# Performance work log

Measured on AMD Instinct MI355X. Metric: run time of the kernel, lower is better.

Reference implementation:

```python
import jax, jax.numpy as jnp
import numpy as np

EPS = 1e-5

def mean_std_norm(x):
    # instance norm without affine: per-(B,C) mean/std over spatial dims
    mean = jnp.mean(x, axis=(2, 3), keepdims=True)
    var = jnp.var(x, axis=(2, 3), keepdims=True)
    return (x - mean) / jnp.sqrt(var + EPS)

def conv1x1(x, w, b):
    # x: [B,C,H,W], w: [O,C], b: [O]
    return jnp.einsum('oc,bchw->bohw', w, x) + b[None, :, None, None]

def setup_inputs() -> dict:
    key = jax.random.key(0)
    ks = jax.random.split(key, 9)
    C = 512
    s = 1.0 / np.sqrt(C)
    inp = {
        'content_feat': jax.random.normal(ks[0], (4, C, 64, 64), dtype=jnp.float32),
        'f_w': jax.random.normal(ks[1], (C, C), dtype=jnp.float32) * s,
        'f_b': jnp.zeros((C,), dtype=jnp.float32),
        'g_w': jax.random.normal(ks[2], (C, C), dtype=jnp.float32) * s,
        'g_b': jnp.zeros((C,), dtype=jnp.float32),
        'h_w': jax.random.normal(ks[3], (C, C), dtype=jnp.float32) * s,
        'h_b': jnp.zeros((C,), dtype=jnp.float32),
        'o_w': jax.random.normal(ks[4], (C, C), dtype=jnp.float32) * s,
        'o_b': jnp.zeros((C,), dtype=jnp.float32),
    }
    return inp

def reference(content_feat, f_w, f_b, g_w, g_b, h_w, h_b, o_w, o_b):
    B, C, H, W = content_feat.shape
    HW = H * W
    norm = mean_std_norm(content_feat)
    # f(norm) -> [B, HW, C]; g(norm) -> [B, C, HW]
    F_Fc = conv1x1(norm, f_w, f_b).reshape(B, C, HW).transpose(0, 2, 1)
    G_Fs = conv1x1(norm, g_w, g_b).reshape(B, C, HW)
    energy = jnp.einsum('bnc,bcm->bnm', F_Fc, G_Fs)  # [B, HW, HW]
    attention = jax.nn.softmax(energy, axis=-1)
    H_Fs = conv1x1(content_feat, h_w, h_b).reshape(B, C, HW)
    # out = H_Fs @ attention^T : out[b,c,m] = sum_n H_Fs[b,c,n] * att[b,m,n]
    out = jnp.einsum('bcn,bmn->bcm', H_Fs, attention).reshape(B, C, H, W)
    out = conv1x1(out, o_w, o_b)
    return out + content_feat
```

## Files before the change

kernel.cpp:

```cpp
#include <hip/hip_runtime.h>


typedef __bf16 bf16_t;
typedef _Float16 f16_t;
typedef _Float16 f16x8 __attribute__((ext_vector_type(8)));
typedef float f32x4 __attribute__((ext_vector_type(4)));

#define LOG2E 1.44269504088896340736f

__device__ __forceinline__ void gload16(const void* g, void* l) {
  __builtin_amdgcn_global_load_lds(
      (const __attribute__((address_space(1))) void*)g,
      (__attribute__((address_space(3))) void*)l, 16, 0, 0);
}

#define WAITV14() asm volatile("s_waitcnt vmcnt(14)" ::: "memory")
#define WAITV10() asm volatile("s_waitcnt vmcnt(10)" ::: "memory")
#define WAITL() asm volatile("s_waitcnt lgkmcnt(0)" ::: "memory")
#define SB() __builtin_amdgcn_s_barrier()
#define SCHED0() __builtin_amdgcn_sched_barrier(0)

__global__ void __launch_bounds__(256) stats_k(const float* __restrict__ x,
                                               float* __restrict__ mu,
                                               float* __restrict__ rs) {
  const int bc = blockIdx.x;
  const float4* row = (const float4*)(x + (size_t)bc * 4096);
  float s = 0.f, ss = 0.f;
  for (int i = threadIdx.x; i < 1024; i += 256) {
    float4 v = row[i];
    s += v.x + v.y + v.z + v.w;
    ss += v.x * v.x + v.y * v.y + v.z * v.z + v.w * v.w;
  }
#pragma unroll
  for (int o = 32; o >= 1; o >>= 1) {
    s += __shfl_down(s, o);
    ss += __shfl_down(ss, o);
  }
  __shared__ float as_[4], ass_[4];
  const int w = threadIdx.x >> 6;
  if ((threadIdx.x & 63) == 0) { as_[w] = s; ass_[w] = ss; }
  __syncthreads();
  if (threadIdx.x == 0) {
    float st = as_[0] + as_[1] + as_[2] + as_[3];
    float sst = ass_[0] + ass_[1] + ass_[2] + ass_[3];
    float m = st * (1.f / 4096.f);
    float var = sst * (1.f / 4096.f) - m * m;
    mu[bc] = m;
    rs[bc] = rsqrtf(var + 1e-5f);
  }
}

__global__ void __launch_bounds__(256) wcast2_k(const float* __restrict__ a,
                                                const float* __restrict__ b,
                                                f16_t* __restrict__ dst) {
  const int i = blockIdx.x * 256 + threadIdx.x;
  const int which = i >> 16;
  const int off = i & 65535;
  const float* s = which ? b : a;
  const float4 v = ((const float4*)s)[off];
  alignas(8) f16_t r[4];
  r[0] = (f16_t)v.x; r[1] = (f16_t)v.y; r[2] = (f16_t)v.z; r[3] = (f16_t)v.w;
  *(uint2*)(dst + ((size_t)which << 18) + (size_t)off * 4) = *(const uint2*)r;
}

__global__ void __launch_bounds__(256) mt_k(const float* __restrict__ fw,
                                            const float* __restrict__ gw,
                                            f16_t* __restrict__ Mh) {
  __shared__ float Fs[32][64];
  __shared__ float Gs[32][64];
  const int t = threadIdx.x;
  const int it = blockIdx.x, jt = blockIdx.y;
  float acc[16];
#pragma unroll
  for (int i = 0; i < 16; ++i) acc[i] = 0.f;
  const int jl = t >> 2, ib = (t & 3) * 16;
  const int lr = t >> 4, lc4 = (t & 15) * 4;
  for (int cc = 0; cc < 16; ++cc) {
    __syncthreads();
#pragma unroll
    for (int rep = 0; rep < 2; ++rep) {
      const int r = lr + rep * 16;
      *(float4*)&Fs[r][lc4] = *(const float4*)(fw + (size_t)(cc * 32 + r) * 512 + it * 64 + lc4);
      *(float4*)&Gs[r][lc4] = *(const float4*)(gw + (size_t)(cc * 32 + r) * 512 + jt * 64 + lc4);
    }
    __syncthreads();
#pragma unroll
    for (int c = 0; c < 32; ++c) {
      const float gv = Gs[c][jl];
#pragma unroll
      for (int ii = 0; ii < 16; ++ii) acc[ii] += gv * Fs[c][ib + ii];
    }
  }
  alignas(16) f16_t hi[16];
#pragma unroll
  for (int ii = 0; ii < 16; ++ii) hi[ii] = (f16_t)acc[ii];
  const size_t o = (size_t)(jt * 64 + jl) * 512 + it * 64 + ib;
  *(uint4*)(Mh + o) = *(const uint4*)hi;
  *(uint4*)(Mh + o + 8) = *(const uint4*)(hi + 8);
}

__global__ void __launch_bounds__(256) v_k(const float* __restrict__ gw,
                                           const float* __restrict__ fb,
                                           float* __restrict__ v) {
  const int j = blockIdx.x * 256 + threadIdx.x;
  float s = 0.f;
  for (int c = 0; c < 512; ++c) s += gw[(size_t)c * 512 + j] * fb[c];
  v[j] = s;
}

__global__ void __launch_bounds__(256) u_k(const float* __restrict__ v,
                                           const f16_t* __restrict__ xf,
                                           float* __restrict__ u) {
  const int w = threadIdx.x >> 6, lane = threadIdx.x & 63;
  const int m = blockIdx.x * 4 + w;
  const int b = blockIdx.y;
  const size_t o = ((size_t)b * 4096 + m) * 512 + lane * 8;
  const f16x8 vh = *(const f16x8*)(xf + o);
  const float4 v0 = *(const float4*)(v + lane * 8);
  const float4 v1 = *(const float4*)(v + lane * 8 + 4);
  float s = 0.f;
  const float* vp = &v0.x;
#pragma unroll
  for (int e = 0; e < 4; ++e) s += (float)vh[e] * vp[e];
  const float* vq = &v1.x;
#pragma unroll
  for (int e = 0; e < 4; ++e) s += (float)vh[4 + e] * vq[e];
#pragma unroll
  for (int o2 = 32; o2 >= 1; o2 >>= 1) s += __shfl_down(s, o2);
  if (lane == 0) u[(size_t)b * 4096 + m] = s;
}

__global__ void __launch_bounds__(256) normt_k(const float* __restrict__ x,
                                               const float* __restrict__ mu,
                                               const float* __restrict__ rs,
                                               f16_t* __restrict__ xf,
                                               f16_t* __restrict__ xc) {
  __shared__ float tile[64][65];
  const int t = threadIdx.x;
  const int nt = blockIdx.x, ct = blockIdx.y, b = blockIdx.z;
  const float* src = x + ((size_t)b * 512 + ct * 64) * 4096 + nt * 64;
  {
    const int r = t >> 4, cq = (t & 15) * 4;
#pragma unroll
    for (int it = 0; it < 4; ++it) {
      const int rr = r + it * 16;
      const float4 v = *(const float4*)(src + (size_t)rr * 4096 + cq);
      tile[rr][cq] = v.x; tile[rr][cq + 1] = v.y;
      tile[rr][cq + 2] = v.z; tile[rr][cq + 3] = v.w;
    }
  }
  __syncthreads();
  const int n = t & 63, ch = t >> 6;
  alignas(16) f16_t vf[16], vc[16];
#pragma unroll
  for (int i = 0; i < 16; ++i) {
    const int c = ch * 16 + i;
    const float v = tile[c][n];
    const int gc = b * 512 + ct * 64 + c;
    vc[i] = (f16_t)v;
    vf[i] = (f16_t)((v - mu[gc]) * rs[gc]);
  }
  const size_t o = ((size_t)b * 4096 + nt * 64 + n) * 512 + ct * 64 + ch * 16;
  *(uint4*)(xf + o) = *(const uint4*)vf;
  *(uint4*)(xf + o + 8) = *(const uint4*)(vf + 8);
  *(uint4*)(xc + o) = *(const uint4*)vc;
  *(uint4*)(xc + o + 8) = *(const uint4*)(vc + 8);
}

template <typename OT, int BIAS, bool RESID>
__global__ void __launch_bounds__(256) gemm_k(const f16_t* __restrict__ A,
                                              const f16_t* __restrict__ Bt,
                                              OT* __restrict__ C,
                                              const float* __restrict__ biasM,
                                              const float* __restrict__ biasN,
                                              const float* __restrict__ resid,
                                              long sAb, long sBb, long sCb, int ldC) {
  __shared__ alignas(16) f16_t As[2][128 * 64];
  __shared__ alignas(16) f16_t Bs[2][128 * 64];
  const int t = threadIdx.x;
  const int lane = t & 63;
  const int w = t >> 6;
  const int wr = w >> 1, wc = w & 1;
  const int l15 = lane & 15, lg = lane >> 4;
  const int b = blockIdx.z;
  const int m0 = blockIdx.y * 128, n0 = blockIdx.x * 128;
  const f16_t* Ab = A + (size_t)sAb * b + (size_t)m0 * 512;
  const f16_t* Bb = Bt + (size_t)sBb * b + (size_t)n0 * 512;
  const int srow = t >> 3;
  const int slot = t & 7;

  auto gstage = [&](int pb_, int ks_) {
#pragma unroll
    for (int r_ = 0; r_ < 4; ++r_) {
      const int rr_ = r_ * 32 + srow;
      const size_t go_ = (size_t)rr_ * 512 + ks_ * 64 + ((slot ^ (rr_ & 7)) * 8);
      gload16(Ab + go_, (char*)As[pb_] + r_ * 4096 + w * 1024);
      gload16(Bb + go_, (char*)Bs[pb_] + r_ * 4096 + w * 1024);
    }
  };

  const f32x4 z4 = {0.f, 0.f, 0.f, 0.f};
  f32x4 acc[4][4];
#pragma unroll
  for (int i = 0; i < 4; ++i)
#pragma unroll
    for (int j = 0; j < 4; ++j) acc[i][j] = z4;

  gstage(0, 0);
  __syncthreads();
  for (int ks = 0; ks < 8; ++ks) {
    const int pb = ks & 1;
    if (ks < 7) gstage(pb ^ 1, ks + 1);
#pragma unroll
    for (int kk = 0; kk < 2; ++kk) {
      f16x8 af[4], bfr[4];
#pragma unroll
      for (int i = 0; i < 4; ++i) {
        const int ra = wr * 64 + i * 16 + l15;
        af[i] = *(const f16x8*)((const char*)As[pb] + ra * 128 + (((kk * 4 + lg) ^ (ra & 7)) * 16));
        const int rb = wc * 64 + i * 16 + l15;
        bfr[i] = *(const f16x8*)((const char*)Bs[pb] + rb * 128 + (((kk * 4 + lg) ^ (rb & 7)) * 16));
      }
#pragma unroll
      for (int i = 0; i < 4; ++i)
#pragma unroll
        for (int j = 0; j < 4; ++j)
          acc[i][j] = __builtin_amdgcn_mfma_f32_16x16x32_f16(af[i], bfr[j], acc[i][j], 0, 0, 0);
    }
    __syncthreads();
  }
  OT* Cb = C + (size_t)sCb * b;
#pragma unroll
  for (int i = 0; i < 4; ++i) {
#pragma unroll
    for (int j = 0; j < 4; ++j) {
      const int n = n0 + wc * 64 + j * 16 + l15;
      float bn = 0.f;
      if (BIAS == 2) bn = biasN[n];
#pragma unroll
      for (int r = 0; r < 4; ++r) {
        const int m = m0 + wr * 64 + i * 16 + lg * 4 + r;
        float v = acc[i][j][r] + bn;
        if (BIAS == 1) v += biasM[m];
        if (RESID) v += resid[(size_t)sCb * b + (size_t)m * ldC + n];
        Cb[(size_t)m * ldC + n] = (OT)v;
      }
    }
  }
}

__global__ void __launch_bounds__(512, 2) flash_k(const f16_t* __restrict__ Z,
                                                  const f16_t* __restrict__ X,
                                                  const float* __restrict__ u,
                                                  const f16_t* __restrict__ Hv,
                                                  f16_t* __restrict__ Oat_t) {
  __shared__ alignas(16) f16_t K[2][64 * 256];
  __shared__ alignas(16) f16_t P[64 * 72];
  __shared__ float redm[4][2][16];
  __shared__ float reds[4][2][16];
  __shared__ float alds[64];
  __shared__ float llds[64];

  const int t = threadIdx.x;
  const int lane = t & 63;
  const int w = t >> 6;
  const int wq = w & 3, wk = w >> 2;
  const int l15 = lane & 15, lg = lane >> 4;
  const int bid = blockIdx.x;
  const int xcd = bid & 7;
  const int b = xcd >> 1;
  const int q0 = ((xcd & 1) * 32 + (bid >> 3)) * 64;

  const f16_t* Kb = X + (size_t)b * 4096 * 512;
  const f16_t* Vb = Hv + (size_t)b * 512 * 4096;
  const float* ub = u + (size_t)b * 4096;

  const int srow = w * 2 + (lane >> 5);
  const int slot32 = lane & 31;

  auto stagek = [&](int pb_, int kt_, int hf_) {
    const int k0_ = kt_ * 64;
#pragma unroll
    for (int r_ = 0; r_ < 4; ++r_) {
      const int row_ = r_ * 16 + srow;
      const size_t go_ = (size_t)(k0_ + row_) * 512 + hf_ * 256 + ((slot32 ^ (row_ & 7)) * 8);
      gload16(Kb + go_, (char*)K[pb_] + r_ * 8192 + w * 1024);
    }
  };

#define QKHALF(PB, HF)                                                                        \
  do {                                                                                        \
    _Pragma("unroll") for (int cwl_ = 0; cwl_ < 8; ++cwl_) {                                  \
      const f16x8 qf_ = qf[(HF) * 8 + cwl_];                                                  \
      _Pragma("unroll") for (int mf_ = 0; mf_ < 2; ++mf_) {                                   \
        const int key_ = 32 * wk + 16 * mf_ + l15;                                            \
        const int so_ = ((cwl_ * 4 + lg) ^ (key_ & 7)) * 16;                                  \
        const f16x8 kf_ = *(const f16x8*)((const char*)K[PB] + key_ * 512 + so_);             \
        sacc[mf_] = __builtin_amdgcn_mfma_f32_16x16x32_f16(kf_, qf_, sacc[mf_], 0, 0, 0);     \
      }                                                                                       \
    }                                                                                         \
  } while (0)

  f16x8 qf[16];
  {
    const size_t qo = ((size_t)b * 4096 + q0 + 16 * wq + l15) * 512 + lg * 8;
#pragma unroll
    for (int cw = 0; cw < 16; ++cw) qf[cw] = *(const f16x8*)(Z + qo + cw * 32);
  }
  stagek(0, 0, 0);
  stagek(1, 0, 1);

  const f32x4 z4 = {0.f, 0.f, 0.f, 0.f};
  f32x4 oacc[4][4];
#pragma unroll
  for (int i = 0; i < 4; ++i)
#pragma unroll
    for (int j = 0; j < 4; ++j) oacc[i][j] = z4;
  float m_run = -3.0e38f, l_run = 0.f;

  for (int kt = 0; kt < 64; ++kt) {
    const int k0 = kt * 64;
    const int ktn = (kt + 1) & 63;
    f32x4 sacc[2] = {z4, z4};
    const float4 u0 = *(const float4*)(ub + k0 + 32 * wk + 4 * lg);
    const float4 u1 = *(const float4*)(ub + k0 + 32 * wk + 16 + 4 * lg);
    f16x8 vpre[4][2];
#pragma unroll
    for (int ct = 0; ct < 4; ++ct) {
      const int c = 64 * w + 16 * ct + l15;
#pragma unroll
      for (int kk = 0; kk < 2; ++kk)
        vpre[ct][kk] = *(const f16x8*)(Vb + (size_t)c * 4096 + k0 + kk * 32 + lg * 8);
    }
    WAITV14(); WAITL(); SB(); SCHED0();
    __builtin_amdgcn_s_setprio(1);
    QKHALF(0, 0);
    __builtin_amdgcn_s_setprio(0);
    WAITL(); WAITV10(); SB(); SCHED0();
    stagek(0, ktn, 0);
    __builtin_amdgcn_s_setprio(1);
    QKHALF(1, 1);
    __builtin_amdgcn_s_setprio(0);
    float pm = -3.0e38f;
    {
      const float* up0 = &u0.x;
      const float* up1 = &u1.x;
#pragma unroll
      for (int j = 0; j < 4; ++j) {
        sacc[0][j] += up0[j];
        sacc[1][j] += up1[j];
        pm = fmaxf(pm, fmaxf(sacc[0][j], sacc[1][j]));
      }
    }
    pm = fmaxf(pm, __shfl_xor(pm, 16));
    pm = fmaxf(pm, __shfl_xor(pm, 32));
    if (lane < 16) redm[wq][wk][lane] = pm;
    WAITL(); SB(); SCHED0();
    stagek(1, ktn, 1);
    const float m_tile = fmaxf(pm, redm[wq][wk ^ 1][l15]);
    float alpha;
    if (m_tile > m_run + 8.f) {
      alpha = exp2f((m_run - m_tile) * LOG2E);
      m_run = m_tile;
    } else {
      alpha = 1.f;
    }
    float ps = 0.f;
    const int qrow = 16 * wq + l15;
    {
      alignas(8) f16_t pk[4];
#pragma unroll
      for (int mf = 0; mf < 2; ++mf) {
#pragma unroll
        for (int j = 0; j < 4; ++j) {
          const float p = exp2f((sacc[mf][j] - m_run) * LOG2E);
          ps += p;
          pk[j] = (f16_t)p;
        }
        *(uint2*)((char*)P + qrow * 144 + 64 * wk + 32 * mf + 8 * lg) = *(const uint2*)pk;
      }
    }
    ps += __shfl_xor(ps, 16);
    ps += __shfl_xor(ps, 32);
    if (lane < 16) {
      reds[wq][wk][lane] = ps;
      if (wk == 0) alds[16 * wq + lane] = alpha;
    }
    WAITL(); SB(); SCHED0();
    const float s_tile = reds[wq][0][l15] + reds[wq][1][l15];
    l_run = l_run * alpha + s_tile;
    float aq[4];
#pragma unroll
    for (int qt = 0; qt < 4; ++qt) aq[qt] = alds[16 * qt + l15];
    const bool need = (aq[0] != 1.f) || (aq[1] != 1.f) || (aq[2] != 1.f) || (aq[3] != 1.f);
    if (__any(need)) {
#pragma unroll
      for (int ct = 0; ct < 4; ++ct)
#pragma unroll
        for (int qt = 0; qt < 4; ++qt) oacc[ct][qt] *= aq[qt];
    }
    __builtin_amdgcn_s_setprio(1);
#pragma unroll
    for (int kk = 0; kk < 2; ++kk) {
      f16x8 bp[4];
#pragma unroll
      for (int qt = 0; qt < 4; ++qt) {
        const int q = 16 * qt + l15;
        bp[qt] = *(const f16x8*)((const char*)P + q * 144 + kk * 64 + lg * 16);
      }
#pragma unroll
      for (int ct = 0; ct < 4; ++ct)
#pragma unroll
        for (int qt = 0; qt < 4; ++qt)
          oacc[ct][qt] =
              __builtin_amdgcn_mfma_f32_16x16x32_f16(vpre[ct][kk], bp[qt], oacc[ct][qt], 0, 0, 0);
    }
    __builtin_amdgcn_s_setprio(0);
  }
#undef QKHALF
  if (wk == 0 && lane < 16) llds[16 * wq + lane] = l_run;
  __syncthreads();
  float inv[4];
#pragma unroll
  for (int qt = 0; qt < 4; ++qt) inv[qt] = 1.f / llds[16 * qt + l15];
#pragma unroll
  for (int ct = 0; ct < 4; ++ct)
#pragma unroll
    for (int qt = 0; qt < 4; ++qt) {
      alignas(8) f16_t o4[4];
#pragma unroll
      for (int j = 0; j < 4; ++j) o4[j] = (f16_t)(oacc[ct][qt][j] * inv[qt]);
      *(uint2*)(Oat_t + ((size_t)b * 4096 + q0 + 16 * qt + l15) * 512 + 64 * w + 16 * ct + 4 * lg) =
          *(const uint2*)o4;
    }
}

extern "C" void kernel_launch(void* const* d_in, const int* in_sizes, int n_in,
                              void* d_out, int out_size, void* d_ws, size_t ws_size,
                              hipStream_t stream) {
  const float* x = (const float*)d_in[0];
  const float* fw = (const float*)d_in[1];
  const float* fb = (const float*)d_in[2];
  const float* gw = (const float*)d_in[3];
  const float* gb = (const float*)d_in[4];
  const float* hw = (const float*)d_in[5];
  const float* hb = (const float*)d_in[6];
  const float* ow = (const float*)d_in[7];
  const float* ob = (const float*)d_in[8];
  float* out = (float*)d_out;
  (void)gb;

  const size_t BIG = (size_t)4 * 4096 * 512 * sizeof(f16_t);
  char* p = (char*)d_ws;
  float* mu = (float*)p; p += 2048 * sizeof(float);
  float* rs = (float*)p; p += 2048 * sizeof(float);
  float* vv = (float*)p; p += 512 * sizeof(float);
  float* uu = (float*)p; p += (size_t)4 * 4096 * sizeof(float);
  f16_t* w2 = (f16_t*)p; p += (size_t)2 * 512 * 512 * sizeof(f16_t);
  f16_t* Mh = (f16_t*)p; p += (size_t)512 * 512 * sizeof(f16_t);
  f16_t* xf = (f16_t*)p; p += BIG;
  f16_t* xc = (f16_t*)p; p += BIG;
  f16_t* Zf = (f16_t*)p; p += BIG;
  f16_t* Hv = (f16_t*)p; p += BIG;
  f16_t* Oat_t = xc;

  f16_t* whb = w2;
  f16_t* wob = w2 + 262144;

  const long sD = (long)4096 * 512;

  stats_k<<<2048, 256, 0, stream>>>(x, mu, rs);
  wcast2_k<<<512, 256, 0, stream>>>(hw, ow, w2);
  mt_k<<<dim3(8, 8), 256, 0, stream>>>(fw, gw, Mh);
  v_k<<<2, 256, 0, stream>>>(gw, fb, vv);
  normt_k<<<dim3(64, 8, 4), 256, 0, stream>>>(x, mu, rs, xf, xc);
  u_k<<<dim3(1024, 4), 256, 0, stream>>>(vv, xf, uu);
  gemm_k<f16_t, 0, false><<<dim3(4, 32, 4), 256, 0, stream>>>(
      xf, Mh, Zf, nullptr, nullptr, nullptr, sD, 0, sD, 512);
  gemm_k<f16_t, 1, false><<<dim3(32, 4, 4), 256, 0, stream>>>(
      whb, xc, Hv, hb, nullptr, nullptr, 0, sD, sD, 4096);
  flash_k<<<256, 512, 0, stream>>>(Zf, xf, uu, Hv, Oat_t);
  gemm_k<float, 1, true><<<dim3(32, 4, 4), 256, 0, stream>>>(
      wob, Oat_t, out, ob, nullptr, x, 0, sD, sD, 4096);

  (void)in_sizes; (void)n_in; (void)out_size; (void)ws_size;
}
```

Measured before the change: 404.1 us.

## Software-pipeline flash attention: overlap QK of tile k with PV of tile k-1

Restructures the flash attention loop so each iteration computes QK^T for the current key tile while doing the P·V MFMAs for the previous tile, using double-buffered P, row-sum and alpha arrays. K staging now loads a whole 64x512 tile per buffer (doubling K LDS) with a single full vmcnt(0) wait per iteration instead of two half-tile waits, which removes one barrier per iteration. A final epilogue drains the last PV tile. The larger LDS footprint (about 140KB) may not allow two blocks per CU, and the full vmcnt(0) wait also waits on the V register loads.

```diff
diff --git a/kernel.cpp b/kernel.cpp
--- a/kernel.cpp
+++ b/kernel.cpp
@@ -14,8 +14,7 @@
       (__attribute__((address_space(3))) void*)l, 16, 0, 0);
 }
 
-#define WAITV14() asm volatile("s_waitcnt vmcnt(14)" ::: "memory")
-#define WAITV10() asm volatile("s_waitcnt vmcnt(10)" ::: "memory")
+#define WAITVL0() asm volatile("s_waitcnt vmcnt(0) lgkmcnt(0)" ::: "memory")
 #define WAITL() asm volatile("s_waitcnt lgkmcnt(0)" ::: "memory")
 #define SB() __builtin_amdgcn_s_barrier()
 #define SCHED0() __builtin_amdgcn_sched_barrier(0)
@@ -254,11 +253,11 @@
                                                   const float* __restrict__ u,
                                                   const f16_t* __restrict__ Hv,
                                                   f16_t* __restrict__ Oat_t) {
-  __shared__ alignas(16) f16_t K[2][64 * 256];
-  __shared__ alignas(16) f16_t P[64 * 72];
+  __shared__ alignas(16) f16_t K[2][64 * 512];
+  __shared__ alignas(16) f16_t P[2][64 * 72];
   __shared__ float redm[4][2][16];
-  __shared__ float reds[4][2][16];
-  __shared__ float alds[64];
+  __shared__ float reds[2][4][2][16];
+  __shared__ float alds[2][64];
   __shared__ float llds[64];
 
   const int t = threadIdx.x;
@@ -275,31 +274,15 @@
   const f16_t* Vb = Hv + (size_t)b * 512 * 4096;
   const float* ub = u + (size_t)b * 4096;
 
-  const int srow = w * 2 + (lane >> 5);
-  const int slot32 = lane & 31;
-
-  auto stagek = [&](int pb_, int kt_, int hf_) {
+  auto stagek = [&](int pb_, int kt_) {
     const int k0_ = kt_ * 64;
 #pragma unroll
-    for (int r_ = 0; r_ < 4; ++r_) {
-      const int row_ = r_ * 16 + srow;
-      const size_t go_ = (size_t)(k0_ + row_) * 512 + hf_ * 256 + ((slot32 ^ (row_ & 7)) * 8);
-      gload16(Kb + go_, (char*)K[pb_] + r_ * 8192 + w * 1024);
+    for (int r_ = 0; r_ < 8; ++r_) {
+      const int row_ = w * 8 + r_;
+      gload16(Kb + (size_t)(k0_ + row_) * 512 + ((lane ^ (row_ & 7)) * 8),
+              (char*)K[pb_] + row_ * 1024);
     }
   };
-
-#define QKHALF(PB, HF)                                                                        \
-  do {                                                                                        \
-    _Pragma("unroll") for (int cwl_ = 0; cwl_ < 8; ++cwl_) {                                  \
-      const f16x8 qf_ = qf[(HF) * 8 + cwl_];                                                  \
-      _Pragma("unroll") for (int mf_ = 0; mf_ < 2; ++mf_) {                                   \
-        const int key_ = 32 * wk + 16 * mf_ + l15;                                            \
-        const int so_ = ((cwl_ * 4 + lg) ^ (key_ & 7)) * 16;                                  \
-        const f16x8 kf_ = *(const f16x8*)((const char*)K[PB] + key_ * 512 + so_);             \
-        sacc[mf_] = __builtin_amdgcn_mfma_f32_16x16x32_f16(kf_, qf_, sacc[mf_], 0, 0, 0);     \
-      }                                                                                       \
-    }                                                                                         \
-  } while (0)
 
   f16x8 qf[16];
   {
@@ -307,8 +290,7 @@
 #pragma unroll
     for (int cw = 0; cw < 16; ++cw) qf[cw] = *(const f16x8*)(Z + qo + cw * 32);
   }
-  stagek(0, 0, 0);
-  stagek(1, 0, 1);
+  stagek(0, 0);
 
   const f32x4 z4 = {0.f, 0.f, 0.f, 0.f};
   f32x4 oacc[4][4];
@@ -316,30 +298,39 @@
   for (int i = 0; i < 4; ++i)
 #pragma unroll
     for (int j = 0; j < 4; ++j) oacc[i][j] = z4;
-  float m_run = -3.0e38f, l_run = 0.f;
-
+  float m_run = -3.0e38f, l_run = 0.f, alpha_prev = 0.f;
+  const int qrow = 16 * wq + l15;
+
+#pragma unroll 2
   for (int kt = 0; kt < 64; ++kt) {
+    const int pb = kt & 1;
     const int k0 = kt * 64;
-    const int ktn = (kt + 1) & 63;
-    f32x4 sacc[2] = {z4, z4};
+    WAITVL0(); SB(); SCHED0();
+    stagek(pb ^ 1, (kt + 1) & 63);
+    const int km1 = (kt + 63) & 63;
+    f16x8 vpre[4][2];
+#pragma unroll
+    for (int ct = 0; ct < 4; ++ct) {
+      const int c = 64 * w + 16 * ct + l15;
+#pragma unroll
+      for (int kk = 0; kk < 2; ++kk)
+        vpre[ct][kk] = *(const f16x8*)(Vb + (size_t)c * 4096 + km1 * 64 + kk * 32 + lg * 8);
+    }
     const float4 u0 = *(const float4*)(ub + k0 + 32 * wk + 4 * lg);
     const float4 u1 = *(const float4*)(ub + k0 + 32 * wk + 16 + 4 * lg);
-    f16x8 vpre[4][2];
-#pragma unroll
-    for (int ct = 0; ct < 4; ++ct) {
-      const int c = 64 * w + 16 * ct + l15;
-#pragma unroll
-      for (int kk = 0; kk < 2; ++kk)
-        vpre[ct][kk] = *(const f16x8*)(Vb + (size_t)c * 4096 + k0 + kk * 32 + lg * 8);
-    }
-    WAITV14(); WAITL(); SB(); SCHED0();
+    f32x4 sacc[2] = {z4, z4};
     __builtin_amdgcn_s_setprio(1);
-    QKHALF(0, 0);
-    __builtin_amdgcn_s_setprio(0);
-    WAITL(); WAITV10(); SB(); SCHED0();
-    stagek(0, ktn, 0);
-    __builtin_amdgcn_s_setprio(1);
-    QKHALF(1, 1);
+#pragma unroll
+    for (int cwl = 0; cwl < 16; ++cwl) {
+      const f16x8 qfv = qf[cwl];
+#pragma unroll
+      for (int mf = 0; mf < 2; ++mf) {
+        const int key = 32 * wk + 16 * mf + l15;
+        const int slot = (cwl * 4 + lg) ^ (key & 7);
+        const f16x8 kf = *(const f16x8*)((const char*)K[pb] + key * 1024 + slot * 16);
+        sacc[mf] = __builtin_amdgcn_mfma_f32_16x16x32_f16(kf, qfv, sacc[mf], 0, 0, 0);
+      }
+    }
     __builtin_amdgcn_s_setprio(0);
     float pm = -3.0e38f;
     {
@@ -355,18 +346,45 @@
     pm = fmaxf(pm, __shfl_xor(pm, 16));
     pm = fmaxf(pm, __shfl_xor(pm, 32));
     if (lane < 16) redm[wq][wk][lane] = pm;
+    if (kt) {
+      float aq[4];
+#pragma unroll
+      for (int qt = 0; qt < 4; ++qt) aq[qt] = alds[pb ^ 1][16 * qt + l15];
+      const bool need = (aq[0] != 1.f) || (aq[1] != 1.f) || (aq[2] != 1.f) || (aq[3] != 1.f);
+      if (__any(need)) {
+#pragma unroll
+        for (int ct = 0; ct < 4; ++ct)
+#pragma unroll
+          for (int qt = 0; qt < 4; ++qt) oacc[ct][qt] *= aq[qt];
+      }
+      __builtin_amdgcn_s_setprio(1);
+#pragma unroll
+      for (int kk = 0; kk < 2; ++kk) {
+        f16x8 bp[4];
+#pragma unroll
+        for (int qt = 0; qt < 4; ++qt) {
+          const int q = 16 * qt + l15;
+          bp[qt] = *(const f16x8*)((const char*)P[pb ^ 1] + q * 144 + kk * 64 + lg * 16);
+        }
+#pragma unroll
+        for (int ct = 0; ct < 4; ++ct)
+#pragma unroll
+          for (int qt = 0; qt < 4; ++qt)
+            oacc[ct][qt] =
+                __builtin_amdgcn_mfma_f32_16x16x32_f16(vpre[ct][kk], bp[qt], oacc[ct][qt], 0, 0, 0);
+      }
+      __builtin_amdgcn_s_setprio(0);
+    }
     WAITL(); SB(); SCHED0();
-    stagek(1, ktn, 1);
+    if (kt) l_run = l_run * alpha_prev + reds[pb ^ 1][wq][0][l15] + reds[pb ^ 1][wq][1][l15];
     const float m_tile = fmaxf(pm, redm[wq][wk ^ 1][l15]);
-    float alpha;
     if (m_tile > m_run + 8.f) {
-      alpha = exp2f((m_run - m_tile) * LOG2E);
+      alpha_prev = exp2f((m_run - m_tile) * LOG2E);
       m_run = m_tile;
     } else {
-      alpha = 1.f;
+      alpha_prev = 1.f;
     }
     float ps = 0.f;
-    const int qrow = 16 * wq + l15;
     {
       alignas(8) f16_t pk[4];
 #pragma unroll
@@ -377,21 +395,22 @@
           ps += p;
           pk[j] = (f16_t)p;
         }
-        *(uint2*)((char*)P + qrow * 144 + 64 * wk + 32 * mf + 8 * lg) = *(const uint2*)pk;
+        *(uint2*)((char*)P[pb] + qrow * 144 + 64 * wk + 32 * mf + 8 * lg) = *(const uint2*)pk;
       }
     }
     ps += __shfl_xor(ps, 16);
     ps += __shfl_xor(ps, 32);
     if (lane < 16) {
-      reds[wq][wk][lane] = ps;
-      if (wk == 0) alds[16 * wq + lane] = alpha;
-    }
-    WAITL(); SB(); SCHED0();
-    const float s_tile = reds[wq][0][l15] + reds[wq][1][l15];
-    l_run = l_run * alpha + s_tile;
+      reds[pb][wq][wk][lane] = ps;
+      if (wk == 0) alds[pb][16 * wq + lane] = alpha_prev;
+    }
+  }
+  WAITL(); SB();
+  l_run = l_run * alpha_prev + reds[1][wq][0][l15] + reds[1][wq][1][l15];
+  {
     float aq[4];
 #pragma unroll
-    for (int qt = 0; qt < 4; ++qt) aq[qt] = alds[16 * qt + l15];
+    for (int qt = 0; qt < 4; ++qt) aq[qt] = alds[1][16 * qt + l15];
     const bool need = (aq[0] != 1.f) || (aq[1] != 1.f) || (aq[2] != 1.f) || (aq[3] != 1.f);
     if (__any(need)) {
 #pragma unroll
@@ -399,25 +418,24 @@
 #pragma unroll
         for (int qt = 0; qt < 4; ++qt) oacc[ct][qt] *= aq[qt];
     }
-    __builtin_amdgcn_s_setprio(1);
 #pragma unroll
     for (int kk = 0; kk < 2; ++kk) {
       f16x8 bp[4];
 #pragma unroll
       for (int qt = 0; qt < 4; ++qt) {
         const int q = 16 * qt + l15;
-        bp[qt] = *(const f16x8*)((const char*)P + q * 144 + kk * 64 + lg * 16);
-      }
-#pragma unroll
-      for (int ct = 0; ct < 4; ++ct)
+        bp[qt] = *(const f16x8*)((const char*)P[1] + q * 144 + kk * 64 + lg * 16);
+      }
+#pragma unroll
+      for (int ct = 0; ct < 4; ++ct) {
+        const int c = 64 * w + 16 * ct + l15;
+        const f16x8 vf = *(const f16x8*)(Vb + (size_t)c * 4096 + 63 * 64 + kk * 32 + lg * 8);
 #pragma unroll
         for (int qt = 0; qt < 4; ++qt)
-          oacc[ct][qt] =
-              __builtin_amdgcn_mfma_f32_16x16x32_f16(vpre[ct][kk], bp[qt], oacc[ct][qt], 0, 0, 0);
-    }
-    __builtin_amdgcn_s_setprio(0);
-  }
-#undef QKHALF
+          oacc[ct][qt] = __builtin_amdgcn_mfma_f32_16x16x32_f16(vf, bp[qt], oacc[ct][qt], 0, 0, 0);
+      }
+    }
+  }
   if (wk == 0 && lane < 16) llds[16 * wq + lane] = l_run;
   __syncthreads();
   float inv[4];
```

After: 576.5 us. 42.6% more time.

## Shrink flash attention tile to 32 queries with 4 waves and single K buffer

Applied to the files above, without the earlier changes.

The flash attention kernel moves from 64-query blocks of 512 threads to 32-query blocks of 256 threads, launching twice as many blocks. The K tile is now held in one 64x512 LDS buffer loaded in a single stage rather than two half-buffers, and each wave owns 128 output channels with V fragments prefetched in two halves. The aim is more blocks for load balance and a simpler stage/wait schedule, at the cost of each K tile being reused by fewer queries, which raises K traffic per block, and of possible lower overlap since the next tile's load is issued only after the QK step.

```diff
diff --git a/kernel.cpp b/kernel.cpp
--- a/kernel.cpp
+++ b/kernel.cpp
@@ -14,7 +14,6 @@
       (__attribute__((address_space(3))) void*)l, 16, 0, 0);
 }
 
-#define WAITV14() asm volatile("s_waitcnt vmcnt(14)" ::: "memory")
 #define WAITV10() asm volatile("s_waitcnt vmcnt(10)" ::: "memory")
 #define WAITL() asm volatile("s_waitcnt lgkmcnt(0)" ::: "memory")
 #define SB() __builtin_amdgcn_s_barrier()
@@ -249,57 +248,41 @@
   }
 }
 
-__global__ void __launch_bounds__(512, 2) flash_k(const f16_t* __restrict__ Z,
+__global__ void __launch_bounds__(256, 1) flash_k(const f16_t* __restrict__ Z,
                                                   const f16_t* __restrict__ X,
                                                   const float* __restrict__ u,
                                                   const f16_t* __restrict__ Hv,
                                                   f16_t* __restrict__ Oat_t) {
-  __shared__ alignas(16) f16_t K[2][64 * 256];
-  __shared__ alignas(16) f16_t P[64 * 72];
-  __shared__ float redm[4][2][16];
-  __shared__ float reds[4][2][16];
-  __shared__ float alds[64];
-  __shared__ float llds[64];
+  __shared__ alignas(16) f16_t K[64 * 512];
+  __shared__ alignas(16) f16_t P[32 * 72];
+  __shared__ float redm[2][2][16];
+  __shared__ float reds[2][2][16];
+  __shared__ float alds[32];
+  __shared__ float llds[32];
 
   const int t = threadIdx.x;
   const int lane = t & 63;
   const int w = t >> 6;
-  const int wq = w & 3, wk = w >> 2;
+  const int wq = w & 1, wk = w >> 1;
   const int l15 = lane & 15, lg = lane >> 4;
   const int bid = blockIdx.x;
   const int xcd = bid & 7;
   const int b = xcd >> 1;
-  const int q0 = ((xcd & 1) * 32 + (bid >> 3)) * 64;
+  const int q0 = ((xcd & 1) * 64 + (bid >> 3)) * 32;
 
   const f16_t* Kb = X + (size_t)b * 4096 * 512;
   const f16_t* Vb = Hv + (size_t)b * 512 * 4096;
   const float* ub = u + (size_t)b * 4096;
 
-  const int srow = w * 2 + (lane >> 5);
-  const int slot32 = lane & 31;
-
-  auto stagek = [&](int pb_, int kt_, int hf_) {
+  auto stagek = [&](int kt_) {
     const int k0_ = kt_ * 64;
 #pragma unroll
-    for (int r_ = 0; r_ < 4; ++r_) {
-      const int row_ = r_ * 16 + srow;
-      const size_t go_ = (size_t)(k0_ + row_) * 512 + hf_ * 256 + ((slot32 ^ (row_ & 7)) * 8);
-      gload16(Kb + go_, (char*)K[pb_] + r_ * 8192 + w * 1024);
+    for (int r_ = 0; r_ < 16; ++r_) {
+      const int row_ = r_ * 4 + w;
+      gload16(Kb + (size_t)(k0_ + row_) * 512 + ((lane ^ (row_ & 7)) * 8),
+              (char*)K + row_ * 1024);
     }
   };
-
-#define QKHALF(PB, HF)                                                                        \
-  do {                                                                                        \
-    _Pragma("unroll") for (int cwl_ = 0; cwl_ < 8; ++cwl_) {                                  \
-      const f16x8 qf_ = qf[(HF) * 8 + cwl_];                                                  \
-      _Pragma("unroll") for (int mf_ = 0; mf_ < 2; ++mf_) {                                   \
-        const int key_ = 32 * wk + 16 * mf_ + l15;                                            \
-        const int so_ = ((cwl_ * 4 + lg) ^ (key_ & 7)) * 16;                                  \
-        const f16x8 kf_ = *(const f16x8*)((const char*)K[PB] + key_ * 512 + so_);             \
-        sacc[mf_] = __builtin_amdgcn_mfma_f32_16x16x32_f16(kf_, qf_, sacc[mf_], 0, 0, 0);     \
-      }                                                                                       \
-    }                                                                                         \
-  } while (0)
 
   f16x8 qf[16];
   {
@@ -307,39 +290,38 @@
 #pragma unroll
     for (int cw = 0; cw < 16; ++cw) qf[cw] = *(const f16x8*)(Z + qo + cw * 32);
   }
-  stagek(0, 0, 0);
-  stagek(1, 0, 1);
+  stagek(0);
 
   const f32x4 z4 = {0.f, 0.f, 0.f, 0.f};
-  f32x4 oacc[4][4];
-#pragma unroll
-  for (int i = 0; i < 4; ++i)
-#pragma unroll
-    for (int j = 0; j < 4; ++j) oacc[i][j] = z4;
+  f32x4 oacc[8][2];
+#pragma unroll
+  for (int i = 0; i < 8; ++i) { oacc[i][0] = z4; oacc[i][1] = z4; }
   float m_run = -3.0e38f, l_run = 0.f;
+  const int qrow = 16 * wq + l15;
+  const int cbase = 128 * w + l15;
 
   for (int kt = 0; kt < 64; ++kt) {
     const int k0 = kt * 64;
-    const int ktn = (kt + 1) & 63;
-    f32x4 sacc[2] = {z4, z4};
     const float4 u0 = *(const float4*)(ub + k0 + 32 * wk + 4 * lg);
     const float4 u1 = *(const float4*)(ub + k0 + 32 * wk + 16 + 4 * lg);
-    f16x8 vpre[4][2];
-#pragma unroll
-    for (int ct = 0; ct < 4; ++ct) {
-      const int c = 64 * w + 16 * ct + l15;
-#pragma unroll
-      for (int kk = 0; kk < 2; ++kk)
-        vpre[ct][kk] = *(const f16x8*)(Vb + (size_t)c * 4096 + k0 + kk * 32 + lg * 8);
-    }
-    WAITV14(); WAITL(); SB(); SCHED0();
+    f16x8 vpre0[8];
+#pragma unroll
+    for (int ct = 0; ct < 8; ++ct)
+      vpre0[ct] = *(const f16x8*)(Vb + (size_t)(cbase + 16 * ct) * 4096 + k0 + lg * 8);
+    WAITV10(); WAITL(); SB(); SCHED0();
+    f32x4 sacc[2] = {z4, z4};
     __builtin_amdgcn_s_setprio(1);
-    QKHALF(0, 0);
-    __builtin_amdgcn_s_setprio(0);
-    WAITL(); WAITV10(); SB(); SCHED0();
-    stagek(0, ktn, 0);
-    __builtin_amdgcn_s_setprio(1);
-    QKHALF(1, 1);
+#pragma unroll
+    for (int cwl = 0; cwl < 16; ++cwl) {
+      const f16x8 qfv = qf[cwl];
+#pragma unroll
+      for (int mf = 0; mf < 2; ++mf) {
+        const int key = 32 * wk + 16 * mf + l15;
+        const int slot = (cwl * 4 + lg) ^ (key & 7);
+        const f16x8 kf = *(const f16x8*)((const char*)K + key * 1024 + slot * 16);
+        sacc[mf] = __builtin_amdgcn_mfma_f32_16x16x32_f16(kf, qfv, sacc[mf], 0, 0, 0);
+      }
+    }
     __builtin_amdgcn_s_setprio(0);
     float pm = -3.0e38f;
     {
@@ -355,8 +337,12 @@
     pm = fmaxf(pm, __shfl_xor(pm, 16));
     pm = fmaxf(pm, __shfl_xor(pm, 32));
     if (lane < 16) redm[wq][wk][lane] = pm;
+    f16x8 vpre1[8];
+#pragma unroll
+    for (int ct = 0; ct < 8; ++ct)
+      vpre1[ct] = *(const f16x8*)(Vb + (size_t)(cbase + 16 * ct) * 4096 + k0 + 32 + lg * 8);
     WAITL(); SB(); SCHED0();
-    stagek(1, ktn, 1);
+    stagek((kt + 1) & 63);
     const float m_tile = fmaxf(pm, redm[wq][wk ^ 1][l15]);
     float alpha;
     if (m_tile > m_run + 8.f) {
@@ -366,7 +352,6 @@
       alpha = 1.f;
     }
     float ps = 0.f;
-    const int qrow = 16 * wq + l15;
     {
       alignas(8) f16_t pk[4];
 #pragma unroll
@@ -387,50 +372,48 @@
       if (wk == 0) alds[16 * wq + lane] = alpha;
     }
     WAITL(); SB(); SCHED0();
-    const float s_tile = reds[wq][0][l15] + reds[wq][1][l15];
-    l_run = l_run * alpha + s_tile;
-    float aq[4];
-#pragma unroll
-    for (int qt = 0; qt < 4; ++qt) aq[qt] = alds[16 * qt + l15];
-    const bool need = (aq[0] != 1.f) || (aq[1] != 1.f) || (aq[2] != 1.f) || (aq[3] != 1.f);
+    l_run = l_run * alpha + reds[wq][0][l15] + reds[wq][1][l15];
+    float aq[2];
+    aq[0] = alds[l15];
+    aq[1] = alds[16 + l15];
+    const bool need = (aq[0] != 1.f) || (aq[1] != 1.f);
     if (__any(need)) {
 #pragma unroll
-      for (int ct = 0; ct < 4; ++ct)
-#pragma unroll
-        for (int qt = 0; qt < 4; ++qt) oacc[ct][qt] *= aq[qt];
+      for (int ct = 0; ct < 8; ++ct) {
+        oacc[ct][0] *= aq[0];
+        oacc[ct][1] *= aq[1];
+      }
     }
     __builtin_amdgcn_s_setprio(1);
 #pragma unroll
     for (int kk = 0; kk < 2; ++kk) {
-      f16x8 bp[4];
-#pragma unroll
-      for (int qt = 0; qt < 4; ++qt) {
-        const int q = 16 * qt + l15;
-        bp[qt] = *(const f16x8*)((const char*)P + q * 144 + kk * 64 + lg * 16);
-      }
-#pragma unroll
-      for (int ct = 0; ct < 4; ++ct)
-#pragma unroll
-        for (int qt = 0; qt < 4; ++qt)
-          oacc[ct][qt] =
-              __builtin_amdgcn_mfma_f32_16x16x32_f16(vpre[ct][kk], bp[qt], oacc[ct][qt], 0, 0, 0);
+      f16x8 bp[2];
+#pragma unroll
+      for (int qt = 0; qt < 2; ++qt)
+        bp[qt] = *(const f16x8*)((const char*)P + (16 * qt + l15) * 144 + kk * 64 + lg * 16);
+#pragma unroll
+      for (int ct = 0; ct < 8; ++ct) {
+        const f16x8 vf = kk ? vpre1[ct] : vpre0[ct];
+#pragma unroll
+        for (int qt = 0; qt < 2; ++qt)
+          oacc[ct][qt] = __builtin_amdgcn_mfma_f32_16x16x32_f16(vf, bp[qt], oacc[ct][qt], 0, 0, 0);
+      }
     }
     __builtin_amdgcn_s_setprio(0);
   }
-#undef QKHALF
   if (wk == 0 && lane < 16) llds[16 * wq + lane] = l_run;
   __syncthreads();
-  float inv[4];
-#pragma unroll
-  for (int qt = 0; qt < 4; ++qt) inv[qt] = 1.f / llds[16 * qt + l15];
-#pragma unroll
-  for (int ct = 0; ct < 4; ++ct)
-#pragma unroll
-    for (int qt = 0; qt < 4; ++qt) {
+  float inv[2];
+  inv[0] = 1.f / llds[l15];
+  inv[1] = 1.f / llds[16 + l15];
+#pragma unroll
+  for (int ct = 0; ct < 8; ++ct)
+#pragma unroll
+    for (int qt = 0; qt < 2; ++qt) {
       alignas(8) f16_t o4[4];
 #pragma unroll
       for (int j = 0; j < 4; ++j) o4[j] = (f16_t)(oacc[ct][qt][j] * inv[qt]);
-      *(uint2*)(Oat_t + ((size_t)b * 4096 + q0 + 16 * qt + l15) * 512 + 64 * w + 16 * ct + 4 * lg) =
+      *(uint2*)(Oat_t + ((size_t)b * 4096 + q0 + 16 * qt + l15) * 512 + 128 * w + 16 * ct + 4 * lg) =
           *(const uint2*)o4;
     }
 }
@@ -479,7 +462,7 @@
       xf, Mh, Zf, nullptr, nullptr, nullptr, sD, 0, sD, 512);
   gemm_k<f16_t, 1, false><<<dim3(32, 4, 4), 256, 0, stream>>>(
       whb, xc, Hv, hb, nullptr, nullptr, 0, sD, sD, 4096);
-  flash_k<<<256, 512, 0, stream>>>(Zf, xf, uu, Hv, Oat_t);
+  flash_k<<<512, 256, 0, stream>>>(Zf, xf, uu, Hv, Oat_t);
   gemm_k<float, 1, true><<<dim3(32, 4, 4), 256, 0, stream>>>(
       wob, Oat_t, out, ob, nullptr, x, 0, sD, sD, 4096);
 
```

Measured after the change: 595.3 us. 1.47x slower.

## Widen flash attention key tile to 128 with full-depth single K buffer

Applied to the files above, without the earlier changes.

The flash attention kernel now processes 128 keys per iteration instead of 64. It stages all 512 channels of the key tile into one 128KB LDS buffer and splits the P·V product into two 64-key halves, so the next tile's K loads and the V register loads interleave with compute. This halves the number of loop iterations and the barrier and softmax-reduction rounds per key. The cost is much more LDS per block, which forces launch bounds to one block per CU, and the LDS wait scheme changes to a single vmcnt(4) wait.

```diff
diff --git a/kernel.cpp b/kernel.cpp
--- a/kernel.cpp
+++ b/kernel.cpp
@@ -14,8 +14,7 @@
       (__attribute__((address_space(3))) void*)l, 16, 0, 0);
 }
 
-#define WAITV14() asm volatile("s_waitcnt vmcnt(14)" ::: "memory")
-#define WAITV10() asm volatile("s_waitcnt vmcnt(10)" ::: "memory")
+#define WAITV4() asm volatile("s_waitcnt vmcnt(4)" ::: "memory")
 #define WAITL() asm volatile("s_waitcnt lgkmcnt(0)" ::: "memory")
 #define SB() __builtin_amdgcn_s_barrier()
 #define SCHED0() __builtin_amdgcn_sched_barrier(0)
@@ -249,13 +248,13 @@
   }
 }
 
-__global__ void __launch_bounds__(512, 2) flash_k(const f16_t* __restrict__ Z,
+__global__ void __launch_bounds__(512, 1) flash_k(const f16_t* __restrict__ Z,
                                                   const f16_t* __restrict__ X,
                                                   const float* __restrict__ u,
                                                   const f16_t* __restrict__ Hv,
                                                   f16_t* __restrict__ Oat_t) {
-  __shared__ alignas(16) f16_t K[2][64 * 256];
-  __shared__ alignas(16) f16_t P[64 * 72];
+  __shared__ alignas(16) f16_t K[128 * 512];
+  __shared__ alignas(16) f16_t P[64 * 136];
   __shared__ float redm[4][2][16];
   __shared__ float reds[4][2][16];
   __shared__ float alds[64];
@@ -275,31 +274,15 @@
   const f16_t* Vb = Hv + (size_t)b * 512 * 4096;
   const float* ub = u + (size_t)b * 4096;
 
-  const int srow = w * 2 + (lane >> 5);
-  const int slot32 = lane & 31;
-
-  auto stagek = [&](int pb_, int kt_, int hf_) {
-    const int k0_ = kt_ * 64;
-#pragma unroll
-    for (int r_ = 0; r_ < 4; ++r_) {
-      const int row_ = r_ * 16 + srow;
-      const size_t go_ = (size_t)(k0_ + row_) * 512 + hf_ * 256 + ((slot32 ^ (row_ & 7)) * 8);
-      gload16(Kb + go_, (char*)K[pb_] + r_ * 8192 + w * 1024);
+  auto stageh = [&](int kt_, int half_) {
+    const int k0_ = kt_ * 128 + half_ * 64;
+#pragma unroll
+    for (int r_ = 0; r_ < 8; ++r_) {
+      const int row_ = half_ * 64 + r_ * 8 + w;
+      gload16(Kb + (size_t)(k0_ + r_ * 8 + w) * 512 + ((lane ^ (row_ & 7)) * 8),
+              (char*)K + row_ * 1024);
     }
   };
-
-#define QKHALF(PB, HF)                                                                        \
-  do {                                                                                        \
-    _Pragma("unroll") for (int cwl_ = 0; cwl_ < 8; ++cwl_) {                                  \
-      const f16x8 qf_ = qf[(HF) * 8 + cwl_];                                                  \
-      _Pragma("unroll") for (int mf_ = 0; mf_ < 2; ++mf_) {                                   \
-        const int key_ = 32 * wk + 16 * mf_ + l15;                                            \
-        const int so_ = ((cwl_ * 4 + lg) ^ (key_ & 7)) * 16;                                  \
-        const f16x8 kf_ = *(const f16x8*)((const char*)K[PB] + key_ * 512 + so_);             \
-        sacc[mf_] = __builtin_amdgcn_mfma_f32_16x16x32_f16(kf_, qf_, sacc[mf_], 0, 0, 0);     \
-      }                                                                                       \
-    }                                                                                         \
-  } while (0)
 
   f16x8 qf[16];
   {
@@ -307,8 +290,8 @@
 #pragma unroll
     for (int cw = 0; cw < 16; ++cw) qf[cw] = *(const f16x8*)(Z + qo + cw * 32);
   }
-  stagek(0, 0, 0);
-  stagek(1, 0, 1);
+  stageh(0, 0);
+  stageh(0, 1);
 
   const f32x4 z4 = {0.f, 0.f, 0.f, 0.f};
   f32x4 oacc[4][4];
@@ -317,46 +300,52 @@
 #pragma unroll
     for (int j = 0; j < 4; ++j) oacc[i][j] = z4;
   float m_run = -3.0e38f, l_run = 0.f;
-
-  for (int kt = 0; kt < 64; ++kt) {
-    const int k0 = kt * 64;
-    const int ktn = (kt + 1) & 63;
-    f32x4 sacc[2] = {z4, z4};
-    const float4 u0 = *(const float4*)(ub + k0 + 32 * wk + 4 * lg);
-    const float4 u1 = *(const float4*)(ub + k0 + 32 * wk + 16 + 4 * lg);
-    f16x8 vpre[4][2];
-#pragma unroll
-    for (int ct = 0; ct < 4; ++ct) {
-      const int c = 64 * w + 16 * ct + l15;
-#pragma unroll
-      for (int kk = 0; kk < 2; ++kk)
-        vpre[ct][kk] = *(const f16x8*)(Vb + (size_t)c * 4096 + k0 + kk * 32 + lg * 8);
-    }
-    WAITV14(); WAITL(); SB(); SCHED0();
+  const int qrow = 16 * wq + l15;
+
+  for (int kt = 0; kt < 32; ++kt) {
+    const int k0 = kt * 128;
+    const int ktn = (kt + 1) & 31;
+    float4 uq[4];
+#pragma unroll
+    for (int mf = 0; mf < 4; ++mf)
+      uq[mf] = *(const float4*)(ub + k0 + 64 * wk + 16 * mf + 4 * lg);
+    WAITV4(); WAITL(); SB(); SCHED0();
+    f32x4 sacc[4] = {z4, z4, z4, z4};
     __builtin_amdgcn_s_setprio(1);
-    QKHALF(0, 0);
-    __builtin_amdgcn_s_setprio(0);
-    WAITL(); WAITV10(); SB(); SCHED0();
-    stagek(0, ktn, 0);
-    __builtin_amdgcn_s_setprio(1);
-    QKHALF(1, 1);
+#pragma unroll
+    for (int cwl = 0; cwl < 16; ++cwl) {
+      const f16x8 qfv = qf[cwl];
+#pragma unroll
+      for (int mf = 0; mf < 4; ++mf) {
+        const int key = 64 * wk + 16 * mf + l15;
+        const int slot = (cwl * 4 + lg) ^ (key & 7);
+        const f16x8 kf = *(const f16x8*)((const char*)K + key * 1024 + slot * 16);
+        sacc[mf] = __builtin_amdgcn_mfma_f32_16x16x32_f16(kf, qfv, sacc[mf], 0, 0, 0);
+      }
+    }
     __builtin_amdgcn_s_setprio(0);
     float pm = -3.0e38f;
-    {
-      const float* up0 = &u0.x;
-      const float* up1 = &u1.x;
+#pragma unroll
+    for (int mf = 0; mf < 4; ++mf) {
+      const float* up = &uq[mf].x;
 #pragma unroll
       for (int j = 0; j < 4; ++j) {
-        sacc[0][j] += up0[j];
-        sacc[1][j] += up1[j];
-        pm = fmaxf(pm, fmaxf(sacc[0][j], sacc[1][j]));
+        sacc[mf][j] += up[j];
+        pm = fmaxf(pm, sacc[mf][j]);
       }
     }
     pm = fmaxf(pm, __shfl_xor(pm, 16));
     pm = fmaxf(pm, __shfl_xor(pm, 32));
     if (lane < 16) redm[wq][wk][lane] = pm;
-    WAITL(); SB(); SCHED0();
-    stagek(1, ktn, 1);
+    WAITL();
+    SB(); SCHED0();
+    f16x8 vA[2][4];
+#pragma unroll
+    for (int kk = 0; kk < 2; ++kk)
+#pragma unroll
+      for (int ct = 0; ct < 4; ++ct)
+        vA[kk][ct] = *(const f16x8*)(Vb + (size_t)(64 * w + 16 * ct + l15) * 4096 + k0 + 32 * kk + 8 * lg);
+    stageh(ktn, 0);
     const float m_tile = fmaxf(pm, redm[wq][wk ^ 1][l15]);
     float alpha;
     if (m_tile > m_run + 8.f) {
@@ -366,18 +355,17 @@
       alpha = 1.f;
     }
     float ps = 0.f;
-    const int qrow = 16 * wq + l15;
     {
       alignas(8) f16_t pk[4];
 #pragma unroll
-      for (int mf = 0; mf < 2; ++mf) {
+      for (int mf = 0; mf < 4; ++mf) {
 #pragma unroll
         for (int j = 0; j < 4; ++j) {
           const float p = exp2f((sacc[mf][j] - m_run) * LOG2E);
           ps += p;
           pk[j] = (f16_t)p;
         }
-        *(uint2*)((char*)P + qrow * 144 + 64 * wk + 32 * mf + 8 * lg) = *(const uint2*)pk;
+        *(uint2*)((char*)P + qrow * 272 + 128 * wk + 32 * mf + 8 * lg) = *(const uint2*)pk;
       }
     }
     ps += __shfl_xor(ps, 16);
@@ -386,9 +374,9 @@
       reds[wq][wk][lane] = ps;
       if (wk == 0) alds[16 * wq + lane] = alpha;
     }
-    WAITL(); SB(); SCHED0();
-    const float s_tile = reds[wq][0][l15] + reds[wq][1][l15];
-    l_run = l_run * alpha + s_tile;
+    WAITL();
+    SB(); SCHED0();
+    l_run = l_run * alpha + reds[wq][0][l15] + reds[wq][1][l15];
     float aq[4];
 #pragma unroll
     for (int qt = 0; qt < 4; ++qt) aq[qt] = alds[16 * qt + l15];
@@ -404,20 +392,39 @@
     for (int kk = 0; kk < 2; ++kk) {
       f16x8 bp[4];
 #pragma unroll
-      for (int qt = 0; qt < 4; ++qt) {
-        const int q = 16 * qt + l15;
-        bp[qt] = *(const f16x8*)((const char*)P + q * 144 + kk * 64 + lg * 16);
-      }
+      for (int qt = 0; qt < 4; ++qt)
+        bp[qt] = *(const f16x8*)((const char*)P + (16 * qt + l15) * 272 + kk * 64 + 16 * lg);
 #pragma unroll
       for (int ct = 0; ct < 4; ++ct)
 #pragma unroll
         for (int qt = 0; qt < 4; ++qt)
           oacc[ct][qt] =
-              __builtin_amdgcn_mfma_f32_16x16x32_f16(vpre[ct][kk], bp[qt], oacc[ct][qt], 0, 0, 0);
+              __builtin_amdgcn_mfma_f32_16x16x32_f16(vA[kk][ct], bp[qt], oacc[ct][qt], 0, 0, 0);
     }
     __builtin_amdgcn_s_setprio(0);
-  }
-#undef QKHALF
+    f16x8 vB[2][4];
+#pragma unroll
+    for (int kk = 0; kk < 2; ++kk)
+#pragma unroll
+      for (int ct = 0; ct < 4; ++ct)
+        vB[kk][ct] = *(const f16x8*)(Vb + (size_t)(64 * w + 16 * ct + l15) * 4096 + k0 + 64 + 32 * kk + 8 * lg);
+    stageh(ktn, 1);
+    __builtin_amdgcn_s_setprio(1);
+#pragma unroll
+    for (int kk = 0; kk < 2; ++kk) {
+      f16x8 bp[4];
+#pragma unroll
+      for (int qt = 0; qt < 4; ++qt)
+        bp[qt] = *(const f16x8*)((const char*)P + (16 * qt + l15) * 272 + (kk + 2) * 64 + 16 * lg);
+#pragma unroll
+      for (int ct = 0; ct < 4; ++ct)
+#pragma unroll
+        for (int qt = 0; qt < 4; ++qt)
+          oacc[ct][qt] =
+              __builtin_amdgcn_mfma_f32_16x16x32_f16(vB[kk][ct], bp[qt], oacc[ct][qt], 0, 0, 0);
+    }
+    __builtin_amdgcn_s_setprio(0);
+  }
   if (wk == 0 && lane < 16) llds[16 * wq + lane] = l_run;
   __syncthreads();
   float inv[4];
```

New measurement: 412.3 us. +2.0%, slower.
